# Kernel tuning notes

Hardware: AMD Instinct MI355X
Metric: run time of the kernel (lower is better)

## Reference

```python
import jax, jax.numpy as jnp
import numpy as np

N, E = 100000, 1600000
IN, HID, NCLS = 128, 128, 64


def setup_inputs() -> dict:
    key = jax.random.key(0)
    ks = jax.random.split(key, 8)
    x = jax.random.normal(ks[0], (N, IN), jnp.float32)
    edge_index = jax.random.randint(ks[1], (2, E), 0, N, dtype=jnp.int32)
    s1 = 1.0 / np.sqrt(IN)
    s2 = 1.0 / np.sqrt(HID)
    return {
        "x": x,
        "edge_index": edge_index,
        "Wl1": jax.random.uniform(ks[2], (IN, HID), jnp.float32, -s1, s1),
        "Wr1": jax.random.uniform(ks[3], (IN, HID), jnp.float32, -s1, s1),
        "b1": jnp.zeros((HID,), jnp.float32),
        "Wl2": jax.random.uniform(ks[4], (HID, NCLS), jnp.float32, -s2, s2),
        "Wr2": jax.random.uniform(ks[5], (HID, NCLS), jnp.float32, -s2, s2),
        "b2": jnp.zeros((NCLS,), jnp.float32),
    }


def _sage_conv(x, src, dst, inv_deg, Wl, Wr, b):
    # mean-aggregate neighbor features at each destination node (PyG SAGEConv)
    agg = jax.ops.segment_sum(x[src], dst, num_segments=N)  # [N, d]
    agg = agg * inv_deg[:, None]
    # out = lin_l(mean_j x_j) + lin_r(x_i); bias lives in lin_l
    return agg @ Wl + x @ Wr + b


def reference(x, edge_index, Wl1, Wr1, b1, Wl2, Wr2, b2):
    src, dst = edge_index[0], edge_index[1]
    deg = jax.ops.segment_sum(jnp.ones((E,), jnp.float32), dst, num_segments=N)
    inv_deg = 1.0 / jnp.maximum(deg, 1.0)
    h = _sage_conv(x, src, dst, inv_deg, Wl1, Wr1, b1)
    h = jax.nn.relu(h)
    # dropout is identity at inference (training=False)
    h = _sage_conv(h, src, dst, inv_deg, Wl2, Wr2, b2)
    return jax.nn.log_softmax(h, axis=1)
```

## Files before the change

### kernel.cpp

```cpp
#include <hip/hip_runtime.h>
#include <hip/hip_bf16.h>


typedef __attribute__((ext_vector_type(8))) short short8;
typedef __attribute__((ext_vector_type(4))) float f32x4;
typedef __attribute__((ext_vector_type(2))) float f32x2;

#define NPB 512
#define BCAP 16384
#define CHUNK 8192

__device__ __forceinline__ ushort f2bf(float f) {
    unsigned u = __float_as_uint(f);
    return (ushort)((u + 0x7fff + ((u >> 16) & 1)) >> 16);
}
__device__ __forceinline__ float bflo(unsigned v) { return __uint_as_float(v << 16); }
__device__ __forceinline__ float bfhi(unsigned v) { return __uint_as_float(v & 0xffff0000u); }
__device__ __forceinline__ unsigned pk4bf(float a, float b) {
    unsigned r;
    asm("v_cvt_pk_bf16_f32 %0, %1, %2" : "=v"(r) : "v"(a), "v"(b));
    return r;
}
__device__ __forceinline__ f32x2 shflx2(f32x2 v, int m) {
    f32x2 r; r[0] = __shfl_xor(v[0], m); r[1] = __shfl_xor(v[1], m); return r;
}

__device__ __forceinline__ void wfrag_one(const float* W, ushort* Wf, int i, int COLS) {
    int j = i & 7, m = (i >> 3) & 15, kc = (i >> 7) & 15, ct = i >> 11;
    Wf[i] = f2bf(W[(kc * 8 + j) * COLS + ct * 16 + m]);
}

__global__ void __launch_bounds__(256)
k1_scatter_cvtw(const int* __restrict__ src, const int* __restrict__ dst,
                int* __restrict__ bcount, unsigned* __restrict__ bbuf, int E, int NSC,
                const float* __restrict__ Wl1, const float* __restrict__ Wr1,
                const float* __restrict__ Wl2, const float* __restrict__ Wr2,
                ushort* __restrict__ Wf_l1, ushort* __restrict__ Wf_r1,
                ushort* __restrict__ Wf_l2, ushort* __restrict__ Wf_r2) {
    int tid = threadIdx.x;
    if ((int)blockIdx.x >= NSC) {
        int i = ((int)blockIdx.x - NSC) * 256 + tid;
        if (i < 16384)       wfrag_one(Wl1, Wf_l1, i, 128);
        else if (i < 32768)  wfrag_one(Wr1, Wf_r1, i - 16384, 128);
        else if (i < 40960)  wfrag_one(Wl2, Wf_l2, i - 32768, 64);
        else if (i < 49152)  wfrag_one(Wr2, Wf_r2, i - 40960, 64);
        return;
    }
    __shared__ unsigned entry[CHUNK];
    __shared__ unsigned char ebkt[CHUNK];
    __shared__ int lhist[256], lbase[256], lcur[256];
    lhist[tid] = 0;
    __syncthreads();
    int e0 = blockIdx.x * CHUNK;
    int cnt = min(CHUNK, E - e0);
    int nv = cnt >> 2;
    for (int t = tid; t < nv; t += 256) {
        int4 d4 = ((const int4*)(dst + e0))[t];
        int4 s4 = ((const int4*)(src + e0))[t];
        int i = t * 4;
        int b0 = d4.x >> 9, b1 = d4.y >> 9, b2 = d4.z >> 9, b3 = d4.w >> 9;
        entry[i + 0] = ((unsigned)s4.x << 9) | (unsigned)(d4.x & 511);
        entry[i + 1] = ((unsigned)s4.y << 9) | (unsigned)(d4.y & 511);
        entry[i + 2] = ((unsigned)s4.z << 9) | (unsigned)(d4.z & 511);
        entry[i + 3] = ((unsigned)s4.w << 9) | (unsigned)(d4.w & 511);
        ebkt[i + 0] = (unsigned char)b0; ebkt[i + 1] = (unsigned char)b1;
        ebkt[i + 2] = (unsigned char)b2; ebkt[i + 3] = (unsigned char)b3;
        atomicAdd(&lhist[b0], 1); atomicAdd(&lhist[b1], 1);
        atomicAdd(&lhist[b2], 1); atomicAdd(&lhist[b3], 1);
    }
    for (int i = (nv << 2) + tid; i < cnt; i += 256) {
        int d = dst[e0 + i], s = src[e0 + i];
        int b = d >> 9;
        entry[i] = ((unsigned)s << 9) | (unsigned)(d & 511);
        ebkt[i] = (unsigned char)b;
        atomicAdd(&lhist[b], 1);
    }
    __syncthreads();
    int h = lhist[tid];
    lbase[tid] = (h > 0) ? atomicAdd(&bcount[tid], h) : 0;
    lcur[tid] = 0;
    __syncthreads();
    for (int i = tid; i < cnt; i += 256) {
        int b = ebkt[i];
        int o = atomicAdd(&lcur[b], 1);
        bbuf[(long)b * BCAP + lbase[b] + o] = entry[i];
    }
}

template <int CTOT>
__device__ __forceinline__ void stage_weights(const ushort* __restrict__ Wfl,
                                              const ushort* __restrict__ Wfr,
                                              ushort* dst, int tid) {
    constexpr int HALF = CTOT / 2;
    constexpr int ITERS = (CTOT * 2) / 8192;
#pragma unroll
    for (int r = 0; r < ITERS; ++r) {
        int u = r * 4096 + tid * 8;
        const ushort* s = (u < HALF) ? (Wfl + u) : (Wfr + (u - HALF));
        *(short8*)(dst + u) = *(const short8*)s;
    }
}

template <int COLS, bool F32IN>
__device__ __forceinline__ void proj_body(int bid, int tid,
                            const void* __restrict__ xin,
                            const ushort* __restrict__ Wfl, const ushort* __restrict__ Wfr,
                            const float* __restrict__ bias,
                            unsigned char* __restrict__ p8, ushort* __restrict__ q, int N,
                            ushort* wsm) {
    constexpr int CT = COLS / 16;
    stage_weights<2 * COLS * 128>(Wfl, Wfr, wsm, tid);
    __syncthreads();
    const ushort* Wl = wsm;
    const ushort* Wr = wsm + COLS * 128;

    int wave = tid >> 6, lane = tid & 63;
    int quad = lane >> 4, m = lane & 15;
    long row0 = (long)bid * 128 + wave * 16;
    long node = row0 + m;
    long arow = (node < N) ? node : (N - 1);

    f32x4 accp[CT], accq[CT];
#pragma unroll
    for (int ct = 0; ct < CT; ++ct) { accp[ct] = (f32x4)0.0f; accq[ct] = (f32x4)0.0f; }

#pragma unroll
    for (int kk = 0; kk < 128; kk += 32) {
        short8 b;
        if (F32IN) {
            const float* xf = (const float*)xin + arow * 128 + kk + quad * 8;
            float4 f0 = *(const float4*)xf;
            float4 f1 = *(const float4*)(xf + 4);
            union { short8 s; unsigned u[4]; } bu;
            bu.u[0] = pk4bf(f0.x, f0.y);
            bu.u[1] = pk4bf(f0.z, f0.w);
            bu.u[2] = pk4bf(f1.x, f1.y);
            bu.u[3] = pk4bf(f1.z, f1.w);
            b = bu.s;
        } else {
            b = *(const short8*)((const ushort*)xin + arow * 128 + kk + quad * 8);
        }
        int kc = (kk >> 3) + quad;
#pragma unroll
        for (int ct = 0; ct < CT; ++ct) {
            int boff = ((ct * 16 + kc) * 16 + m) * 8;
            short8 al = *(const short8*)(Wl + boff);
            short8 ar = *(const short8*)(Wr + boff);
            accp[ct] = __builtin_amdgcn_mfma_f32_16x16x32_bf16(al, b, accp[ct], 0, 0, 0);
            accq[ct] = __builtin_amdgcn_mfma_f32_16x16x32_bf16(ar, b, accq[ct], 0, 0, 0);
        }
    }

    if (node <= N) {
        unsigned msk = (node == N) ? 0u : ~0u;
#pragma unroll
        for (int ct = 0; ct < CT; ++ct) {
            int c0 = ct * 16 + quad * 4;
            float4 bv = *(const float4*)(bias + c0);
            float q0 = accq[ct][0] + bv.x, q1 = accq[ct][1] + bv.y;
            float q2 = accq[ct][2] + bv.z, q3 = accq[ct][3] + bv.w;
            unsigned w = (unsigned)__builtin_amdgcn_cvt_pk_fp8_f32(accp[ct][0], accp[ct][1], 0, false);
            w = (unsigned)__builtin_amdgcn_cvt_pk_fp8_f32(accp[ct][2], accp[ct][3], (int)w, true);
            *(unsigned*)(p8 + node * COLS + c0) = w & msk;
            uint2 qw; qw.x = pk4bf(q0, q1) & msk; qw.y = pk4bf(q2, q3) & msk;
            *(uint2*)(q + node * COLS + c0) = qw;
        }
    }
}

__global__ void __launch_bounds__(512, 4)
k2_csr_proj1(const unsigned* __restrict__ bbuf, const int* __restrict__ bcount,
             int* __restrict__ rsd,
             float* __restrict__ inv_deg, int* __restrict__ ssrc, int NBcsr, int N,
             const float* __restrict__ x,
             const ushort* __restrict__ Wfl, const ushort* __restrict__ Wfr,
             const float* __restrict__ bias,
             unsigned char* __restrict__ p8, ushort* __restrict__ q) {
    extern __shared__ char smem[];
    int tid = threadIdx.x;
    if ((int)blockIdx.x >= NBcsr) {
        proj_body<128, true>((int)blockIdx.x - NBcsr, tid, x, Wfl, Wfr, bias, p8, q, N,
                             (ushort*)smem);
        return;
    }
    int* sdeg = (int*)smem;
    int* lcur = sdeg + NPB;
    int* wsum = lcur + NPB;
    int b = blockIdx.x;
    int node0 = b * NPB;
    sdeg[tid] = 0;
    __syncthreads();
    int cnt = bcount[b];
    long base = (long)b * BCAP;
    const unsigned* bb = bbuf + base;
    int nv = cnt >> 2;
    for (int t = tid; t < nv; t += 512) {
        uint4 e = ((const uint4*)bb)[t];
        atomicAdd(&sdeg[e.x & 511], 1);
        atomicAdd(&sdeg[e.y & 511], 1);
        atomicAdd(&sdeg[e.z & 511], 1);
        atomicAdd(&sdeg[e.w & 511], 1);
    }
    for (int i = (nv << 2) + tid; i < cnt; i += 512)
        atomicAdd(&sdeg[bb[i] & 511], 1);
    __syncthreads();
    int lane = tid & 63, wv = tid >> 6;
    int c0 = sdeg[tid];
    int dp = (c0 + 15) & ~15;
    int v = dp;
#pragma unroll
    for (int o = 1; o < 64; o <<= 1) {
        int t = __shfl_up(v, o);
        if (lane >= o) v += t;
    }
    if (lane == 63) wsum[wv] = v;
    __syncthreads();
    int add = 0;
    for (int w = 0; w < wv; ++w) add += wsum[w];
    int rs0 = v + add - dp;
    lcur[tid] = rs0;
    if (node0 + tid < N) {
        int2 rv; rv.x = (int)(base + rs0); rv.y = dp;
        *(int2*)(rsd + 2 * (node0 + tid)) = rv;
        inv_deg[node0 + tid] = 1.0f / (float)(c0 > 1 ? c0 : 1);
    }
    __syncthreads();
    for (int t = tid; t < nv; t += 512) {
        uint4 e = ((const uint4*)bb)[t];
        int p0 = atomicAdd(&lcur[e.x & 511], 1);
        int p1 = atomicAdd(&lcur[e.y & 511], 1);
        int p2 = atomicAdd(&lcur[e.z & 511], 1);
        int p3 = atomicAdd(&lcur[e.w & 511], 1);
        ssrc[base + p0] = (int)(e.x >> 9);
        ssrc[base + p1] = (int)(e.y >> 9);
        ssrc[base + p2] = (int)(e.z >> 9);
        ssrc[base + p3] = (int)(e.w >> 9);
    }
    for (int i = (nv << 2) + tid; i < cnt; i += 512) {
        unsigned w = bb[i];
        int pos = atomicAdd(&lcur[w & 511], 1);
        ssrc[base + pos] = (int)(w >> 9);
    }
    for (int i = c0; i < dp; ++i) ssrc[base + rs0 + i] = N;
    if (tid == 511) {
        int tot = v + add;
        for (int k = 0; k < 16; ++k) ssrc[base + tot + k] = N;
    }
}

__global__ void __launch_bounds__(256)
agg_relu_kernel(const unsigned char* __restrict__ p8,
                const ushort* __restrict__ q,
                const int* __restrict__ ssrc,
                const int* __restrict__ rsd,
                const float* __restrict__ inv_deg,
                ushort* __restrict__ hb, int N) {
    int wave = threadIdx.x >> 6, lane = threadIdx.x & 63;
    int n = blockIdx.x * 4 + wave;
    if (n >= N) return;
    int g = lane >> 4, lm = lane & 15;
    int2 rv = *(const int2*)(rsd + 2 * n);
    int start = rv.x, dp = rv.y;
    float iv = inv_deg[n];
    uint4 qv = make_uint4(0u, 0u, 0u, 0u);
    if (g == 0) qv = *(const uint4*)(q + (long)n * 128 + lm * 8);
    const int* sp = ssrc + start;
    const unsigned char* pb = p8 + lm * 8;
    f32x2 a0 = (f32x2)0.f, a1 = (f32x2)0.f, a2 = (f32x2)0.f, a3 = (f32x2)0.f;
    int4 s = *(const int4*)(sp + 4 * g);
    for (int j = 0; j < dp; j += 16) {
        uint2 v0 = *(const uint2*)(pb + (unsigned)s.x * 128u);
        uint2 v1 = *(const uint2*)(pb + (unsigned)s.y * 128u);
        uint2 v2 = *(const uint2*)(pb + (unsigned)s.z * 128u);
        uint2 v3 = *(const uint2*)(pb + (unsigned)s.w * 128u);
        s = *(const int4*)(sp + j + 16 + 4 * g);
        a0 += __builtin_amdgcn_cvt_pk_f32_fp8((int)v0.x, false);
        a1 += __builtin_amdgcn_cvt_pk_f32_fp8((int)v0.x, true);
        a2 += __builtin_amdgcn_cvt_pk_f32_fp8((int)v0.y, false);
        a3 += __builtin_amdgcn_cvt_pk_f32_fp8((int)v0.y, true);
        a0 += __builtin_amdgcn_cvt_pk_f32_fp8((int)v1.x, false);
        a1 += __builtin_amdgcn_cvt_pk_f32_fp8((int)v1.x, true);
        a2 += __builtin_amdgcn_cvt_pk_f32_fp8((int)v1.y, false);
        a3 += __builtin_amdgcn_cvt_pk_f32_fp8((int)v1.y, true);
        a0 += __builtin_amdgcn_cvt_pk_f32_fp8((int)v2.x, false);
        a1 += __builtin_amdgcn_cvt_pk_f32_fp8((int)v2.x, true);
        a2 += __builtin_amdgcn_cvt_pk_f32_fp8((int)v2.y, false);
        a3 += __builtin_amdgcn_cvt_pk_f32_fp8((int)v2.y, true);
        a0 += __builtin_amdgcn_cvt_pk_f32_fp8((int)v3.x, false);
        a1 += __builtin_amdgcn_cvt_pk_f32_fp8((int)v3.x, true);
        a2 += __builtin_amdgcn_cvt_pk_f32_fp8((int)v3.y, false);
        a3 += __builtin_amdgcn_cvt_pk_f32_fp8((int)v3.y, true);
    }
    a0 += shflx2(a0, 16); a1 += shflx2(a1, 16);
    a2 += shflx2(a2, 16); a3 += shflx2(a3, 16);
    a0 += shflx2(a0, 32); a1 += shflx2(a1, 32);
    a2 += shflx2(a2, 32); a3 += shflx2(a3, 32);
    if (g == 0) {
        float h0 = fmaxf(a0[0] * iv + bflo(qv.x), 0.f);
        float h1 = fmaxf(a0[1] * iv + bfhi(qv.x), 0.f);
        float h2 = fmaxf(a1[0] * iv + bflo(qv.y), 0.f);
        float h3 = fmaxf(a1[1] * iv + bfhi(qv.y), 0.f);
        float h4 = fmaxf(a2[0] * iv + bflo(qv.z), 0.f);
        float h5 = fmaxf(a2[1] * iv + bfhi(qv.z), 0.f);
        float h6 = fmaxf(a3[0] * iv + bflo(qv.w), 0.f);
        float h7 = fmaxf(a3[1] * iv + bfhi(qv.w), 0.f);
        uint4 hw;
        hw.x = pk4bf(h0, h1); hw.y = pk4bf(h2, h3);
        hw.z = pk4bf(h4, h5); hw.w = pk4bf(h6, h7);
        *(uint4*)(hb + (long)n * 128 + lm * 8) = hw;
    }
}

__global__ void __launch_bounds__(512, 4)
proj2_kernel(const ushort* __restrict__ hb,
             const ushort* __restrict__ Wfl, const ushort* __restrict__ Wfr,
             const float* __restrict__ bias,
             unsigned char* __restrict__ u8, ushort* __restrict__ v, int N) {
    __shared__ ushort wsm[2 * 64 * 128];
    proj_body<64, false>((int)blockIdx.x, (int)threadIdx.x, hb, Wfl, Wfr, bias, u8, v, N,
                         wsm);
}

__global__ void __launch_bounds__(256)
agg_lsm_kernel(const unsigned char* __restrict__ u8,
               const ushort* __restrict__ v,
               const int* __restrict__ ssrc,
               const int* __restrict__ rsd,
               const float* __restrict__ inv_deg,
               float* __restrict__ out, int N) {
    int wave = threadIdx.x >> 6, lane = threadIdx.x & 63;
    int n = blockIdx.x * 4 + wave;
    if (n >= N) return;
    int g = lane >> 4, lm = lane & 15;
    int2 rv = *(const int2*)(rsd + 2 * n);
    int start = rv.x, dp = rv.y;
    float iv = inv_deg[n];
    uint2 vv2 = *(const uint2*)(v + (long)n * 64 + lm * 4);
    const int* sp = ssrc + start;
    const unsigned char* ub = u8 + lm * 4;
    f32x2 a0 = (f32x2)0.f, a1 = (f32x2)0.f;
    int4 s = *(const int4*)(sp + 4 * g);
    for (int j = 0; j < dp; j += 16) {
        unsigned v0 = *(const unsigned*)(ub + (unsigned)s.x * 64u);
        unsigned v1 = *(const unsigned*)(ub + (unsigned)s.y * 64u);
        unsigned v2 = *(const unsigned*)(ub + (unsigned)s.z * 64u);
        unsigned v3 = *(const unsigned*)(ub + (unsigned)s.w * 64u);
        s = *(const int4*)(sp + j + 16 + 4 * g);
        a0 += __builtin_amdgcn_cvt_pk_f32_fp8((int)v0, false);
        a1 += __builtin_amdgcn_cvt_pk_f32_fp8((int)v0, true);
        a0 += __builtin_amdgcn_cvt_pk_f32_fp8((int)v1, false);
        a1 += __builtin_amdgcn_cvt_pk_f32_fp8((int)v1, true);
        a0 += __builtin_amdgcn_cvt_pk_f32_fp8((int)v2, false);
        a1 += __builtin_amdgcn_cvt_pk_f32_fp8((int)v2, true);
        a0 += __builtin_amdgcn_cvt_pk_f32_fp8((int)v3, false);
        a1 += __builtin_amdgcn_cvt_pk_f32_fp8((int)v3, true);
    }
    a0 += shflx2(a0, 16); a1 += shflx2(a1, 16);
    a0 += shflx2(a0, 32); a1 += shflx2(a1, 32);

    float z0 = a0[0] * iv + bflo(vv2.x), z1 = a0[1] * iv + bfhi(vv2.x);
    float z2 = a1[0] * iv + bflo(vv2.y), z3 = a1[1] * iv + bfhi(vv2.y);
    float mx = fmaxf(fmaxf(z0, z1), fmaxf(z2, z3));
#pragma unroll
    for (int o = 8; o > 0; o >>= 1) mx = fmaxf(mx, __shfl_xor(mx, o));
    float e = (__expf(z0 - mx) + __expf(z1 - mx)) + (__expf(z2 - mx) + __expf(z3 - mx));
#pragma unroll
    for (int o = 8; o > 0; o >>= 1) e += __shfl_xor(e, o);
    float ls = mx + __logf(e);
    if (g == 0) {
        float4 o0;
        o0.x = z0 - ls; o0.y = z1 - ls; o0.z = z2 - ls; o0.w = z3 - ls;
        *(float4*)(out + (long)n * 64 + lm * 4) = o0;
    }
}

extern "C" void kernel_launch(void* const* d_in, const int* in_sizes, int n_in,
                              void* d_out, int out_size, void* d_ws, size_t ws_size,
                              hipStream_t stream) {
    const float* x   = (const float*)d_in[0];
    const int*   ei  = (const int*)d_in[1];
    const float* Wl1 = (const float*)d_in[2];
    const float* Wr1 = (const float*)d_in[3];
    const float* b1  = (const float*)d_in[4];
    const float* Wl2 = (const float*)d_in[5];
    const float* Wr2 = (const float*)d_in[6];
    const float* b2  = (const float*)d_in[7];

    const int N = in_sizes[0] / 128;
    const int E = in_sizes[1] / 2;
    const int* src = ei;
    const int* dst = ei + E;
    const int NB = (N + NPB - 1) / NPB;
    const int NSC = (E + CHUNK - 1) / CHUNK;

    size_t off = 0;
    auto take = [&](size_t nbytes) -> void* {
        void* ptr = (void*)((char*)d_ws + off);
        off += (nbytes + 255) & ~(size_t)255;
        return ptr;
    };
    int*      bcount    = (int*)take((size_t)NB * 4);
    unsigned* bbuf      = (unsigned*)take((size_t)NB * BCAP * 4);
    int*      rsd       = (int*)take((size_t)N * 8);
    float*    inv_deg   = (float*)take((size_t)N * 4);
    int*      ssrc      = (int*)take((size_t)NB * BCAP * 4);
    unsigned char* p8   = (unsigned char*)take((size_t)(N + 1) * 128);
    ushort*   q         = (ushort*)take((size_t)(N + 1) * 128 * 2);
    ushort*   hb        = (ushort*)take((size_t)N * 128 * 2);
    ushort*   Wf_l1     = (ushort*)take(128 * 128 * 2);
    ushort*   Wf_r1     = (ushort*)take(128 * 128 * 2);
    ushort*   Wf_l2     = (ushort*)take(64 * 128 * 2);
    ushort*   Wf_r2     = (ushort*)take(64 * 128 * 2);
    unsigned char* u8 = p8;
    ushort*        v  = q;
    (void)ws_size; (void)n_in; (void)out_size;

    static bool attr_set = false;
    if (!attr_set) {
        hipFuncSetAttribute((const void*)k2_csr_proj1,
                            hipFuncAttributeMaxDynamicSharedMemorySize, 65536);
        attr_set = true;
    }

    hipMemsetAsync(bcount, 0, (size_t)NB * 4, stream);

    k1_scatter_cvtw<<<NSC + 192, 256, 0, stream>>>(src, dst, bcount, bbuf, E, NSC,
                                                   Wl1, Wr1, Wl2, Wr2,
                                                   Wf_l1, Wf_r1, Wf_l2, Wf_r2);

    int P1 = (N + 127) / 128;
    k2_csr_proj1<<<NB + P1, 512, 65536, stream>>>(bbuf, bcount, rsd, inv_deg,
                                                  ssrc, NB, N, x, Wf_l1, Wf_r1, b1, p8, q);

    agg_relu_kernel<<<(N + 3) / 4, 256, 0, stream>>>(p8, q, ssrc, rsd, inv_deg, hb, N);

    proj2_kernel<<<(N + 127) / 128, 512, 0, stream>>>(hb, Wf_l2, Wf_r2, b2, u8, v, N);
    agg_lsm_kernel<<<(N + 3) / 4, 256, 0, stream>>>(u8, v, ssrc, rsd, inv_deg,
                                                    (float*)d_out, N);
}
```

Baseline: 242.9 us.

## Process two nodes per wave in aggregation kernels and cache bucket edges in LDS

Both aggregation kernels now give each wave two destination nodes and interleave their gathers, so twice as many independent memory requests are in flight per wave, and launch half as many blocks. The CSR build kernel keeps the bucket's edges in shared memory during the degree-count pass, so the scatter pass reads them from LDS instead of global memory again. The cost is more registers per wave, an imbalance tail when the two nodes have different degrees, and LDS space near the 64 KB dynamic limit.

```diff
diff --git a/kernel.cpp b/kernel.cpp
--- a/kernel.cpp
+++ b/kernel.cpp
@@ -186,6 +186,8 @@
     int* sdeg = (int*)smem;
     int* lcur = sdeg + NPB;
     int* wsum = lcur + NPB;
+    unsigned* ecache = (unsigned*)(wsum + 16);
+    const int ECAPV = 3836;
     int b = blockIdx.x;
     int node0 = b * NPB;
     sdeg[tid] = 0;
@@ -194,8 +196,10 @@
     long base = (long)b * BCAP;
     const unsigned* bb = bbuf + base;
     int nv = cnt >> 2;
+    int cnv = min(nv, ECAPV);
     for (int t = tid; t < nv; t += 512) {
         uint4 e = ((const uint4*)bb)[t];
+        if (t < cnv) ((uint4*)ecache)[t] = e;
         atomicAdd(&sdeg[e.x & 511], 1);
         atomicAdd(&sdeg[e.y & 511], 1);
         atomicAdd(&sdeg[e.z & 511], 1);
@@ -225,7 +229,18 @@
         inv_deg[node0 + tid] = 1.0f / (float)(c0 > 1 ? c0 : 1);
     }
     __syncthreads();
-    for (int t = tid; t < nv; t += 512) {
+    for (int t = tid; t < cnv; t += 512) {
+        uint4 e = ((const uint4*)ecache)[t];
+        int p0 = atomicAdd(&lcur[e.x & 511], 1);
+        int p1 = atomicAdd(&lcur[e.y & 511], 1);
+        int p2 = atomicAdd(&lcur[e.z & 511], 1);
+        int p3 = atomicAdd(&lcur[e.w & 511], 1);
+        ssrc[base + p0] = (int)(e.x >> 9);
+        ssrc[base + p1] = (int)(e.y >> 9);
+        ssrc[base + p2] = (int)(e.z >> 9);
+        ssrc[base + p3] = (int)(e.w >> 9);
+    }
+    for (int t = cnv + tid; t < nv; t += 512) {
         uint4 e = ((const uint4*)bb)[t];
         int p0 = atomicAdd(&lcur[e.x & 511], 1);
         int p1 = atomicAdd(&lcur[e.y & 511], 1);
@@ -256,58 +271,155 @@
                 const float* __restrict__ inv_deg,
                 ushort* __restrict__ hb, int N) {
     int wave = threadIdx.x >> 6, lane = threadIdx.x & 63;
-    int n = blockIdx.x * 4 + wave;
-    if (n >= N) return;
+    int nA = blockIdx.x * 8 + wave * 2;
+    if (nA >= N) return;
+    int nB = nA + 1;
+    bool hasB = (nB < N);
     int g = lane >> 4, lm = lane & 15;
-    int2 rv = *(const int2*)(rsd + 2 * n);
-    int start = rv.x, dp = rv.y;
-    float iv = inv_deg[n];
-    uint4 qv = make_uint4(0u, 0u, 0u, 0u);
-    if (g == 0) qv = *(const uint4*)(q + (long)n * 128 + lm * 8);
-    const int* sp = ssrc + start;
+    int2 rvA = *(const int2*)(rsd + 2 * nA);
+    int2 rvB = hasB ? *(const int2*)(rsd + 2 * nB) : make_int2(rvA.x, 0);
+    int dpA = rvA.y, dpB = rvB.y;
+    float ivA = inv_deg[nA];
+    float ivB = hasB ? inv_deg[nB] : 0.f;
+    uint4 qvA = make_uint4(0u,0u,0u,0u), qvB = make_uint4(0u,0u,0u,0u);
+    if (g == 0) {
+        qvA = *(const uint4*)(q + (long)nA * 128 + lm * 8);
+        if (hasB) qvB = *(const uint4*)(q + (long)nB * 128 + lm * 8);
+    }
+    const int* spA = ssrc + rvA.x;
+    const int* spB = ssrc + rvB.x;
     const unsigned char* pb = p8 + lm * 8;
-    f32x2 a0 = (f32x2)0.f, a1 = (f32x2)0.f, a2 = (f32x2)0.f, a3 = (f32x2)0.f;
-    int4 s = *(const int4*)(sp + 4 * g);
-    for (int j = 0; j < dp; j += 16) {
-        uint2 v0 = *(const uint2*)(pb + (unsigned)s.x * 128u);
-        uint2 v1 = *(const uint2*)(pb + (unsigned)s.y * 128u);
-        uint2 v2 = *(const uint2*)(pb + (unsigned)s.z * 128u);
-        uint2 v3 = *(const uint2*)(pb + (unsigned)s.w * 128u);
-        s = *(const int4*)(sp + j + 16 + 4 * g);
-        a0 += __builtin_amdgcn_cvt_pk_f32_fp8((int)v0.x, false);
-        a1 += __builtin_amdgcn_cvt_pk_f32_fp8((int)v0.x, true);
-        a2 += __builtin_amdgcn_cvt_pk_f32_fp8((int)v0.y, false);
-        a3 += __builtin_amdgcn_cvt_pk_f32_fp8((int)v0.y, true);
-        a0 += __builtin_amdgcn_cvt_pk_f32_fp8((int)v1.x, false);
-        a1 += __builtin_amdgcn_cvt_pk_f32_fp8((int)v1.x, true);
-        a2 += __builtin_amdgcn_cvt_pk_f32_fp8((int)v1.y, false);
-        a3 += __builtin_amdgcn_cvt_pk_f32_fp8((int)v1.y, true);
-        a0 += __builtin_amdgcn_cvt_pk_f32_fp8((int)v2.x, false);
-        a1 += __builtin_amdgcn_cvt_pk_f32_fp8((int)v2.x, true);
-        a2 += __builtin_amdgcn_cvt_pk_f32_fp8((int)v2.y, false);
-        a3 += __builtin_amdgcn_cvt_pk_f32_fp8((int)v2.y, true);
-        a0 += __builtin_amdgcn_cvt_pk_f32_fp8((int)v3.x, false);
-        a1 += __builtin_amdgcn_cvt_pk_f32_fp8((int)v3.x, true);
-        a2 += __builtin_amdgcn_cvt_pk_f32_fp8((int)v3.y, false);
-        a3 += __builtin_amdgcn_cvt_pk_f32_fp8((int)v3.y, true);
-    }
-    a0 += shflx2(a0, 16); a1 += shflx2(a1, 16);
-    a2 += shflx2(a2, 16); a3 += shflx2(a3, 16);
-    a0 += shflx2(a0, 32); a1 += shflx2(a1, 32);
-    a2 += shflx2(a2, 32); a3 += shflx2(a3, 32);
+    f32x2 aA0=(f32x2)0.f, aA1=(f32x2)0.f, aA2=(f32x2)0.f, aA3=(f32x2)0.f;
+    f32x2 aB0=(f32x2)0.f, aB1=(f32x2)0.f, aB2=(f32x2)0.f, aB3=(f32x2)0.f;
+    int4 sA = *(const int4*)(spA + 4 * g);
+    int4 sB = *(const int4*)(spB + 4 * g);
+    int dmin = min(dpA, dpB);
+    int j = 0;
+    for (; j < dmin; j += 16) {
+        uint2 a0 = *(const uint2*)(pb + (unsigned)sA.x * 128u);
+        uint2 a1 = *(const uint2*)(pb + (unsigned)sA.y * 128u);
+        uint2 a2 = *(const uint2*)(pb + (unsigned)sA.z * 128u);
+        uint2 a3 = *(const uint2*)(pb + (unsigned)sA.w * 128u);
+        uint2 b0 = *(const uint2*)(pb + (unsigned)sB.x * 128u);
+        uint2 b1 = *(const uint2*)(pb + (unsigned)sB.y * 128u);
+        uint2 b2 = *(const uint2*)(pb + (unsigned)sB.z * 128u);
+        uint2 b3 = *(const uint2*)(pb + (unsigned)sB.w * 128u);
+        sA = *(const int4*)(spA + j + 16 + 4 * g);
+        sB = *(const int4*)(spB + j + 16 + 4 * g);
+        aA0 += __builtin_amdgcn_cvt_pk_f32_fp8((int)a0.x, false);
+        aA1 += __builtin_amdgcn_cvt_pk_f32_fp8((int)a0.x, true);
+        aA2 += __builtin_amdgcn_cvt_pk_f32_fp8((int)a0.y, false);
+        aA3 += __builtin_amdgcn_cvt_pk_f32_fp8((int)a0.y, true);
+        aA0 += __builtin_amdgcn_cvt_pk_f32_fp8((int)a1.x, false);
+        aA1 += __builtin_amdgcn_cvt_pk_f32_fp8((int)a1.x, true);
+        aA2 += __builtin_amdgcn_cvt_pk_f32_fp8((int)a1.y, false);
+        aA3 += __builtin_amdgcn_cvt_pk_f32_fp8((int)a1.y, true);
+        aA0 += __builtin_amdgcn_cvt_pk_f32_fp8((int)a2.x, false);
+        aA1 += __builtin_amdgcn_cvt_pk_f32_fp8((int)a2.x, true);
+        aA2 += __builtin_amdgcn_cvt_pk_f32_fp8((int)a2.y, false);
+        aA3 += __builtin_amdgcn_cvt_pk_f32_fp8((int)a2.y, true);
+        aA0 += __builtin_amdgcn_cvt_pk_f32_fp8((int)a3.x, false);
+        aA1 += __builtin_amdgcn_cvt_pk_f32_fp8((int)a3.x, true);
+        aA2 += __builtin_amdgcn_cvt_pk_f32_fp8((int)a3.y, false);
+        aA3 += __builtin_amdgcn_cvt_pk_f32_fp8((int)a3.y, true);
+        aB0 += __builtin_amdgcn_cvt_pk_f32_fp8((int)b0.x, false);
+        aB1 += __builtin_amdgcn_cvt_pk_f32_fp8((int)b0.x, true);
+        aB2 += __builtin_amdgcn_cvt_pk_f32_fp8((int)b0.y, false);
+        aB3 += __builtin_amdgcn_cvt_pk_f32_fp8((int)b0.y, true);
+        aB0 += __builtin_amdgcn_cvt_pk_f32_fp8((int)b1.x, false);
+        aB1 += __builtin_amdgcn_cvt_pk_f32_fp8((int)b1.x, true);
+        aB2 += __builtin_amdgcn_cvt_pk_f32_fp8((int)b1.y, false);
+        aB3 += __builtin_amdgcn_cvt_pk_f32_fp8((int)b1.y, true);
+        aB0 += __builtin_amdgcn_cvt_pk_f32_fp8((int)b2.x, false);
+        aB1 += __builtin_amdgcn_cvt_pk_f32_fp8((int)b2.x, true);
+        aB2 += __builtin_amdgcn_cvt_pk_f32_fp8((int)b2.y, false);
+        aB3 += __builtin_amdgcn_cvt_pk_f32_fp8((int)b2.y, true);
+        aB0 += __builtin_amdgcn_cvt_pk_f32_fp8((int)b3.x, false);
+        aB1 += __builtin_amdgcn_cvt_pk_f32_fp8((int)b3.x, true);
+        aB2 += __builtin_amdgcn_cvt_pk_f32_fp8((int)b3.y, false);
+        aB3 += __builtin_amdgcn_cvt_pk_f32_fp8((int)b3.y, true);
+    }
+    for (; j < dpA; j += 16) {
+        uint2 a0 = *(const uint2*)(pb + (unsigned)sA.x * 128u);
+        uint2 a1 = *(const uint2*)(pb + (unsigned)sA.y * 128u);
+        uint2 a2 = *(const uint2*)(pb + (unsigned)sA.z * 128u);
+        uint2 a3 = *(const uint2*)(pb + (unsigned)sA.w * 128u);
+        sA = *(const int4*)(spA + j + 16 + 4 * g);
+        aA0 += __builtin_amdgcn_cvt_pk_f32_fp8((int)a0.x, false);
+        aA1 += __builtin_amdgcn_cvt_pk_f32_fp8((int)a0.x, true);
+        aA2 += __builtin_amdgcn_cvt_pk_f32_fp8((int)a0.y, false);
+        aA3 += __builtin_amdgcn_cvt_pk_f32_fp8((int)a0.y, true);
+        aA0 += __builtin_amdgcn_cvt_pk_f32_fp8((int)a1.x, false);
+        aA1 += __builtin_amdgcn_cvt_pk_f32_fp8((int)a1.x, true);
+        aA2 += __builtin_amdgcn_cvt_pk_f32_fp8((int)a1.y, false);
+        aA3 += __builtin_amdgcn_cvt_pk_f32_fp8((int)a1.y, true);
+        aA0 += __builtin_amdgcn_cvt_pk_f32_fp8((int)a2.x, false);
+        aA1 += __builtin_amdgcn_cvt_pk_f32_fp8((int)a2.x, true);
+        aA2 += __builtin_amdgcn_cvt_pk_f32_fp8((int)a2.y, false);
+        aA3 += __builtin_amdgcn_cvt_pk_f32_fp8((int)a2.y, true);
+        aA0 += __builtin_amdgcn_cvt_pk_f32_fp8((int)a3.x, false);
+        aA1 += __builtin_amdgcn_cvt_pk_f32_fp8((int)a3.x, true);
+        aA2 += __builtin_amdgcn_cvt_pk_f32_fp8((int)a3.y, false);
+        aA3 += __builtin_amdgcn_cvt_pk_f32_fp8((int)a3.y, true);
+    }
+    for (; j < dpB; j += 16) {
+        uint2 b0 = *(const uint2*)(pb + (unsigned)sB.x * 128u);
+        uint2 b1 = *(const uint2*)(pb + (unsigned)sB.y * 128u);
+        uint2 b2 = *(const uint2*)(pb + (unsigned)sB.z * 128u);
+        uint2 b3 = *(const uint2*)(pb + (unsigned)sB.w * 128u);
+        sB = *(const int4*)(spB + j + 16 + 4 * g);
+        aB0 += __builtin_amdgcn_cvt_pk_f32_fp8((int)b0.x, false);
+        aB1 += __builtin_amdgcn_cvt_pk_f32_fp8((int)b0.x, true);
+        aB2 += __builtin_amdgcn_cvt_pk_f32_fp8((int)b0.y, false);
+        aB3 += __builtin_amdgcn_cvt_pk_f32_fp8((int)b0.y, true);
+        aB0 += __builtin_amdgcn_cvt_pk_f32_fp8((int)b1.x, false);
+        aB1 += __builtin_amdgcn_cvt_pk_f32_fp8((int)b1.x, true);
+        aB2 += __builtin_amdgcn_cvt_pk_f32_fp8((int)b1.y, false);
+        aB3 += __builtin_amdgcn_cvt_pk_f32_fp8((int)b1.y, true);
+        aB0 += __builtin_amdgcn_cvt_pk_f32_fp8((int)b2.x, false);
+        aB1 += __builtin_amdgcn_cvt_pk_f32_fp8((int)b2.x, true);
+        aB2 += __builtin_amdgcn_cvt_pk_f32_fp8((int)b2.y, false);
+        aB3 += __builtin_amdgcn_cvt_pk_f32_fp8((int)b2.y, true);
+        aB0 += __builtin_amdgcn_cvt_pk_f32_fp8((int)b3.x, false);
+        aB1 += __builtin_amdgcn_cvt_pk_f32_fp8((int)b3.x, true);
+        aB2 += __builtin_amdgcn_cvt_pk_f32_fp8((int)b3.y, false);
+        aB3 += __builtin_amdgcn_cvt_pk_f32_fp8((int)b3.y, true);
+    }
+    aA0 += shflx2(aA0, 16); aA1 += shflx2(aA1, 16);
+    aA2 += shflx2(aA2, 16); aA3 += shflx2(aA3, 16);
+    aB0 += shflx2(aB0, 16); aB1 += shflx2(aB1, 16);
+    aB2 += shflx2(aB2, 16); aB3 += shflx2(aB3, 16);
+    aA0 += shflx2(aA0, 32); aA1 += shflx2(aA1, 32);
+    aA2 += shflx2(aA2, 32); aA3 += shflx2(aA3, 32);
+    aB0 += shflx2(aB0, 32); aB1 += shflx2(aB1, 32);
+    aB2 += shflx2(aB2, 32); aB3 += shflx2(aB3, 32);
     if (g == 0) {
-        float h0 = fmaxf(a0[0] * iv + bflo(qv.x), 0.f);
-        float h1 = fmaxf(a0[1] * iv + bfhi(qv.x), 0.f);
-        float h2 = fmaxf(a1[0] * iv + bflo(qv.y), 0.f);
-        float h3 = fmaxf(a1[1] * iv + bfhi(qv.y), 0.f);
-        float h4 = fmaxf(a2[0] * iv + bflo(qv.z), 0.f);
-        float h5 = fmaxf(a2[1] * iv + bfhi(qv.z), 0.f);
-        float h6 = fmaxf(a3[0] * iv + bflo(qv.w), 0.f);
-        float h7 = fmaxf(a3[1] * iv + bfhi(qv.w), 0.f);
+        float h0 = fmaxf(aA0[0] * ivA + bflo(qvA.x), 0.f);
+        float h1 = fmaxf(aA0[1] * ivA + bfhi(qvA.x), 0.f);
+        float h2 = fmaxf(aA1[0] * ivA + bflo(qvA.y), 0.f);
+        float h3 = fmaxf(aA1[1] * ivA + bfhi(qvA.y), 0.f);
+        float h4 = fmaxf(aA2[0] * ivA + bflo(qvA.z), 0.f);
+        float h5 = fmaxf(aA2[1] * ivA + bfhi(qvA.z), 0.f);
+        float h6 = fmaxf(aA3[0] * ivA + bflo(qvA.w), 0.f);
+        float h7 = fmaxf(aA3[1] * ivA + bfhi(qvA.w), 0.f);
         uint4 hw;
         hw.x = pk4bf(h0, h1); hw.y = pk4bf(h2, h3);
         hw.z = pk4bf(h4, h5); hw.w = pk4bf(h6, h7);
-        *(uint4*)(hb + (long)n * 128 + lm * 8) = hw;
+        *(uint4*)(hb + (long)nA * 128 + lm * 8) = hw;
+        if (hasB) {
+            float g0 = fmaxf(aB0[0] * ivB + bflo(qvB.x), 0.f);
+            float g1 = fmaxf(aB0[1] * ivB + bfhi(qvB.x), 0.f);
+            float g2 = fmaxf(aB1[0] * ivB + bflo(qvB.y), 0.f);
+            float g3 = fmaxf(aB1[1] * ivB + bfhi(qvB.y), 0.f);
+            float g4 = fmaxf(aB2[0] * ivB + bflo(qvB.z), 0.f);
+            float g5 = fmaxf(aB2[1] * ivB + bfhi(qvB.z), 0.f);
+            float g6 = fmaxf(aB3[0] * ivB + bflo(qvB.w), 0.f);
+            float g7 = fmaxf(aB3[1] * ivB + bfhi(qvB.w), 0.f);
+            uint4 gw;
+            gw.x = pk4bf(g0, g1); gw.y = pk4bf(g2, g3);
+            gw.z = pk4bf(g4, g5); gw.w = pk4bf(g6, g7);
+            *(uint4*)(hb + (long)nB * 128 + lm * 8) = gw;
+        }
     }
 }
 
@@ -329,48 +441,118 @@
                const float* __restrict__ inv_deg,
                float* __restrict__ out, int N) {
     int wave = threadIdx.x >> 6, lane = threadIdx.x & 63;
-    int n = blockIdx.x * 4 + wave;
-    if (n >= N) return;
+    int nA = blockIdx.x * 8 + wave * 2;
+    if (nA >= N) return;
+    int nB = nA + 1;
+    bool hasB = (nB < N);
     int g = lane >> 4, lm = lane & 15;
-    int2 rv = *(const int2*)(rsd + 2 * n);
-    int start = rv.x, dp = rv.y;
-    float iv = inv_deg[n];
-    uint2 vv2 = *(const uint2*)(v + (long)n * 64 + lm * 4);
-    const int* sp = ssrc + start;
+    int2 rvA = *(const int2*)(rsd + 2 * nA);
+    int2 rvB = hasB ? *(const int2*)(rsd + 2 * nB) : make_int2(rvA.x, 0);
+    int dpA = rvA.y, dpB = rvB.y;
+    float ivA = inv_deg[nA];
+    float ivB = hasB ? inv_deg[nB] : 0.f;
+    uint2 vvA = *(const uint2*)(v + (long)nA * 64 + lm * 4);
+    uint2 vvB = hasB ? *(const uint2*)(v + (long)nB * 64 + lm * 4) : make_uint2(0u,0u);
+    const int* spA = ssrc + rvA.x;
+    const int* spB = ssrc + rvB.x;
     const unsigned char* ub = u8 + lm * 4;
-    f32x2 a0 = (f32x2)0.f, a1 = (f32x2)0.f;
-    int4 s = *(const int4*)(sp + 4 * g);
-    for (int j = 0; j < dp; j += 16) {
-        unsigned v0 = *(const unsigned*)(ub + (unsigned)s.x * 64u);
-        unsigned v1 = *(const unsigned*)(ub + (unsigned)s.y * 64u);
-        unsigned v2 = *(const unsigned*)(ub + (unsigned)s.z * 64u);
-        unsigned v3 = *(const unsigned*)(ub + (unsigned)s.w * 64u);
-        s = *(const int4*)(sp + j + 16 + 4 * g);
-        a0 += __builtin_amdgcn_cvt_pk_f32_fp8((int)v0, false);
-        a1 += __builtin_amdgcn_cvt_pk_f32_fp8((int)v0, true);
-        a0 += __builtin_amdgcn_cvt_pk_f32_fp8((int)v1, false);
-        a1 += __builtin_amdgcn_cvt_pk_f32_fp8((int)v1, true);
-        a0 += __builtin_amdgcn_cvt_pk_f32_fp8((int)v2, false);
-        a1 += __builtin_amdgcn_cvt_pk_f32_fp8((int)v2, true);
-        a0 += __builtin_amdgcn_cvt_pk_f32_fp8((int)v3, false);
-        a1 += __builtin_amdgcn_cvt_pk_f32_fp8((int)v3, true);
-    }
-    a0 += shflx2(a0, 16); a1 += shflx2(a1, 16);
-    a0 += shflx2(a0, 32); a1 += shflx2(a1, 32);
-
-    float z0 = a0[0] * iv + bflo(vv2.x), z1 = a0[1] * iv + bfhi(vv2.x);
-    float z2 = a1[0] * iv + bflo(vv2.y), z3 = a1[1] * iv + bfhi(vv2.y);
-    float mx = fmaxf(fmaxf(z0, z1), fmaxf(z2, z3));
-#pragma unroll
-    for (int o = 8; o > 0; o >>= 1) mx = fmaxf(mx, __shfl_xor(mx, o));
-    float e = (__expf(z0 - mx) + __expf(z1 - mx)) + (__expf(z2 - mx) + __expf(z3 - mx));
-#pragma unroll
-    for (int o = 8; o > 0; o >>= 1) e += __shfl_xor(e, o);
-    float ls = mx + __logf(e);
+    f32x2 aA0=(f32x2)0.f, aA1=(f32x2)0.f, aB0=(f32x2)0.f, aB1=(f32x2)0.f;
+    int4 sA = *(const int4*)(spA + 4 * g);
+    int4 sB = *(const int4*)(spB + 4 * g);
+    int dmin = min(dpA, dpB);
+    int j = 0;
+    for (; j < dmin; j += 16) {
+        unsigned a0 = *(const unsigned*)(ub + (unsigned)sA.x * 64u);
+        unsigned a1 = *(const unsigned*)(ub + (unsigned)sA.y * 64u);
+        unsigned a2 = *(const unsigned*)(ub + (unsigned)sA.z * 64u);
+        unsigned a3 = *(const unsigned*)(ub + (unsigned)sA.w * 64u);
+        unsigned b0 = *(const unsigned*)(ub + (unsigned)sB.x * 64u);
+        unsigned b1 = *(const unsigned*)(ub + (unsigned)sB.y * 64u);
+        unsigned b2 = *(const unsigned*)(ub + (unsigned)sB.z * 64u);
+        unsigned b3 = *(const unsigned*)(ub + (unsigned)sB.w * 64u);
+        sA = *(const int4*)(spA + j + 16 + 4 * g);
+        sB = *(const int4*)(spB + j + 16 + 4 * g);
+        aA0 += __builtin_amdgcn_cvt_pk_f32_fp8((int)a0, false);
+        aA1 += __builtin_amdgcn_cvt_pk_f32_fp8((int)a0, true);
+        aA0 += __builtin_amdgcn_cvt_pk_f32_fp8((int)a1, false);
+        aA1 += __builtin_amdgcn_cvt_pk_f32_fp8((int)a1, true);
+        aA0 += __builtin_amdgcn_cvt_pk_f32_fp8((int)a2, false);
+        aA1 += __builtin_amdgcn_cvt_pk_f32_fp8((int)a2, true);
+        aA0 += __builtin_amdgcn_cvt_pk_f32_fp8((int)a3, false);
+        aA1 += __builtin_amdgcn_cvt_pk_f32_fp8((int)a3, true);
+        aB0 += __builtin_amdgcn_cvt_pk_f32_fp8((int)b0, false);
+        aB1 += __builtin_amdgcn_cvt_pk_f32_fp8((int)b0, true);
+        aB0 += __builtin_amdgcn_cvt_pk_f32_fp8((int)b1, false);
+        aB1 += __builtin_amdgcn_cvt_pk_f32_fp8((int)b1, true);
+        aB0 += __builtin_amdgcn_cvt_pk_f32_fp8((int)b2, false);
+        aB1 += __builtin_amdgcn_cvt_pk_f32_fp8((int)b2, true);
+        aB0 += __builtin_amdgcn_cvt_pk_f32_fp8((int)b3, false);
+        aB1 += __builtin_amdgcn_cvt_pk_f32_fp8((int)b3, true);
+    }
+    for (; j < dpA; j += 16) {
+        unsigned a0 = *(const unsigned*)(ub + (unsigned)sA.x * 64u);
+        unsigned a1 = *(const unsigned*)(ub + (unsigned)sA.y * 64u);
+        unsigned a2 = *(const unsigned*)(ub + (unsigned)sA.z * 64u);
+        unsigned a3 = *(const unsigned*)(ub + (unsigned)sA.w * 64u);
+        sA = *(const int4*)(spA + j + 16 + 4 * g);
+        aA0 += __builtin_amdgcn_cvt_pk_f32_fp8((int)a0, false);
+        aA1 += __builtin_amdgcn_cvt_pk_f32_fp8((int)a0, true);
+        aA0 += __builtin_amdgcn_cvt_pk_f32_fp8((int)a1, false);
+        aA1 += __builtin_amdgcn_cvt_pk_f32_fp8((int)a1, true);
+        aA0 += __builtin_amdgcn_cvt_pk_f32_fp8((int)a2, false);
+        aA1 += __builtin_amdgcn_cvt_pk_f32_fp8((int)a2, true);
+        aA0 += __builtin_amdgcn_cvt_pk_f32_fp8((int)a3, false);
+        aA1 += __builtin_amdgcn_cvt_pk_f32_fp8((int)a3, true);
+    }
+    for (; j < dpB; j += 16) {
+        unsigned b0 = *(const unsigned*)(ub + (unsigned)sB.x * 64u);
+        unsigned b1 = *(const unsigned*)(ub + (unsigned)sB.y * 64u);
+        unsigned b2 = *(const unsigned*)(ub + (unsigned)sB.z * 64u);
+        unsigned b3 = *(const unsigned*)(ub + (unsigned)sB.w * 64u);
+        sB = *(const int4*)(spB + j + 16 + 4 * g);
+        aB0 += __builtin_amdgcn_cvt_pk_f32_fp8((int)b0, false);
+        aB1 += __builtin_amdgcn_cvt_pk_f32_fp8((int)b0, true);
+        aB0 += __builtin_amdgcn_cvt_pk_f32_fp8((int)b1, false);
+        aB1 += __builtin_amdgcn_cvt_pk_f32_fp8((int)b1, true);
+        aB0 += __builtin_amdgcn_cvt_pk_f32_fp8((int)b2, false);
+        aB1 += __builtin_amdgcn_cvt_pk_f32_fp8((int)b2, true);
+        aB0 += __builtin_amdgcn_cvt_pk_f32_fp8((int)b3, false);
+        aB1 += __builtin_amdgcn_cvt_pk_f32_fp8((int)b3, true);
+    }
+    aA0 += shflx2(aA0, 16); aA1 += shflx2(aA1, 16);
+    aB0 += shflx2(aB0, 16); aB1 += shflx2(aB1, 16);
+    aA0 += shflx2(aA0, 32); aA1 += shflx2(aA1, 32);
+    aB0 += shflx2(aB0, 32); aB1 += shflx2(aB1, 32);
+
+    float zA0 = aA0[0] * ivA + bflo(vvA.x), zA1 = aA0[1] * ivA + bfhi(vvA.x);
+    float zA2 = aA1[0] * ivA + bflo(vvA.y), zA3 = aA1[1] * ivA + bfhi(vvA.y);
+    float zB0 = aB0[0] * ivB + bflo(vvB.x), zB1 = aB0[1] * ivB + bfhi(vvB.x);
+    float zB2 = aB1[0] * ivB + bflo(vvB.y), zB3 = aB1[1] * ivB + bfhi(vvB.y);
+    float mA = fmaxf(fmaxf(zA0, zA1), fmaxf(zA2, zA3));
+    float mB = fmaxf(fmaxf(zB0, zB1), fmaxf(zB2, zB3));
+#pragma unroll
+    for (int o = 8; o > 0; o >>= 1) {
+        mA = fmaxf(mA, __shfl_xor(mA, o));
+        mB = fmaxf(mB, __shfl_xor(mB, o));
+    }
+    float eA = (__expf(zA0 - mA) + __expf(zA1 - mA)) + (__expf(zA2 - mA) + __expf(zA3 - mA));
+    float eB = (__expf(zB0 - mB) + __expf(zB1 - mB)) + (__expf(zB2 - mB) + __expf(zB3 - mB));
+#pragma unroll
+    for (int o = 8; o > 0; o >>= 1) {
+        eA += __shfl_xor(eA, o);
+        eB += __shfl_xor(eB, o);
+    }
+    float lsA = mA + __logf(eA);
+    float lsB = mB + __logf(eB);
     if (g == 0) {
-        float4 o0;
-        o0.x = z0 - ls; o0.y = z1 - ls; o0.z = z2 - ls; o0.w = z3 - ls;
-        *(float4*)(out + (long)n * 64 + lm * 4) = o0;
+        float4 oA;
+        oA.x = zA0 - lsA; oA.y = zA1 - lsA; oA.z = zA2 - lsA; oA.w = zA3 - lsA;
+        *(float4*)(out + (long)nA * 64 + lm * 4) = oA;
+        if (hasB) {
+            float4 oB;
+            oB.x = zB0 - lsB; oB.y = zB1 - lsB; oB.z = zB2 - lsB; oB.w = zB3 - lsB;
+            *(float4*)(out + (long)nB * 64 + lm * 4) = oB;
+        }
     }
 }
 
@@ -432,9 +614,9 @@
     k2_csr_proj1<<<NB + P1, 512, 65536, stream>>>(bbuf, bcount, rsd, inv_deg,
                                                   ssrc, NB, N, x, Wf_l1, Wf_r1, b1, p8, q);
 
-    agg_relu_kernel<<<(N + 3) / 4, 256, 0, stream>>>(p8, q, ssrc, rsd, inv_deg, hb, N);
+    agg_relu_kernel<<<(N + 7) / 8, 256, 0, stream>>>(p8, q, ssrc, rsd, inv_deg, hb, N);
 
     proj2_kernel<<<(N + 127) / 128, 512, 0, stream>>>(hb, Wf_l2, Wf_r2, b2, u8, v, N);
-    agg_lsm_kernel<<<(N + 3) / 4, 256, 0, stream>>>(u8, v, ssrc, rsd, inv_deg,
+    agg_lsm_kernel<<<(N + 7) / 8, 256, 0, stream>>>(u8, v, ssrc, rsd, inv_deg,
                                                     (float*)d_out, N);
 }
```

New measurement: 242.4 us. No clear change (-0.2%).

## Persist proj1 blocks, cache CSR edges in LDS, use packed f32 adds

Applied to the files above, without the earlier changes.

The projection part of k2 becomes a persistent grid of 316 blocks. Each block stages the bf16 weights into shared memory once and then loops over row tiles, instead of restaging per 128-row tile. The CSR build blocks keep up to about 15K edges in the unused LDS during the degree pass, so the scatter pass reads them from LDS instead of re-reading global memory. Both aggregation kernels now accumulate with an explicit v_pk_add_f32 in inline asm. The risks are less scheduling freedom for the compiler around the asm and load imbalance across the persistent blocks.

```diff
diff --git a/kernel.cpp b/kernel.cpp
--- a/kernel.cpp
+++ b/kernel.cpp
@@ -19,6 +19,11 @@
 __device__ __forceinline__ unsigned pk4bf(float a, float b) {
     unsigned r;
     asm("v_cvt_pk_bf16_f32 %0, %1, %2" : "=v"(r) : "v"(a), "v"(b));
+    return r;
+}
+__device__ __forceinline__ f32x2 pkadd(f32x2 a, f32x2 b) {
+    f32x2 r;
+    asm("v_pk_add_f32 %0, %1, %2" : "=v"(r) : "v"(a), "v"(b));
     return r;
 }
 __device__ __forceinline__ f32x2 shflx2(f32x2 v, int m) {
@@ -102,18 +107,12 @@
 }
 
 template <int COLS, bool F32IN>
-__device__ __forceinline__ void proj_body(int bid, int tid,
+__device__ __forceinline__ void proj_tile(int bid, int tid,
                             const void* __restrict__ xin,
-                            const ushort* __restrict__ Wfl, const ushort* __restrict__ Wfr,
+                            const ushort* Wl, const ushort* Wr,
                             const float* __restrict__ bias,
-                            unsigned char* __restrict__ p8, ushort* __restrict__ q, int N,
-                            ushort* wsm) {
+                            unsigned char* __restrict__ p8, ushort* __restrict__ q, int N) {
     constexpr int CT = COLS / 16;
-    stage_weights<2 * COLS * 128>(Wfl, Wfr, wsm, tid);
-    __syncthreads();
-    const ushort* Wl = wsm;
-    const ushort* Wr = wsm + COLS * 128;
-
     int wave = tid >> 6, lane = tid & 63;
     int quad = lane >> 4, m = lane & 15;
     long row0 = (long)bid * 128 + wave * 16;
@@ -171,7 +170,8 @@
 __global__ void __launch_bounds__(512, 4)
 k2_csr_proj1(const unsigned* __restrict__ bbuf, const int* __restrict__ bcount,
              int* __restrict__ rsd,
-             float* __restrict__ inv_deg, int* __restrict__ ssrc, int NBcsr, int N,
+             float* __restrict__ inv_deg, int* __restrict__ ssrc,
+             int NBcsr, int PGRID, int NT, int N,
              const float* __restrict__ x,
              const ushort* __restrict__ Wfl, const ushort* __restrict__ Wfr,
              const float* __restrict__ bias,
@@ -179,13 +179,18 @@
     extern __shared__ char smem[];
     int tid = threadIdx.x;
     if ((int)blockIdx.x >= NBcsr) {
-        proj_body<128, true>((int)blockIdx.x - NBcsr, tid, x, Wfl, Wfr, bias, p8, q, N,
-                             (ushort*)smem);
+        ushort* wsm = (ushort*)smem;
+        stage_weights<2 * 128 * 128>(Wfl, Wfr, wsm, tid);
+        __syncthreads();
+        for (int t = (int)blockIdx.x - NBcsr; t < NT; t += PGRID)
+            proj_tile<128, true>(t, tid, x, wsm, wsm + 128 * 128, bias, p8, q, N);
         return;
     }
     int* sdeg = (int*)smem;
     int* lcur = sdeg + NPB;
     int* wsum = lcur + NPB;
+    unsigned* ecache = (unsigned*)(wsum + 16);
+    const int ECAPV = 3836;
     int b = blockIdx.x;
     int node0 = b * NPB;
     sdeg[tid] = 0;
@@ -194,8 +199,10 @@
     long base = (long)b * BCAP;
     const unsigned* bb = bbuf + base;
     int nv = cnt >> 2;
+    int cnv = min(nv, ECAPV);
     for (int t = tid; t < nv; t += 512) {
         uint4 e = ((const uint4*)bb)[t];
+        if (t < cnv) ((uint4*)ecache)[t] = e;
         atomicAdd(&sdeg[e.x & 511], 1);
         atomicAdd(&sdeg[e.y & 511], 1);
         atomicAdd(&sdeg[e.z & 511], 1);
@@ -225,7 +232,18 @@
         inv_deg[node0 + tid] = 1.0f / (float)(c0 > 1 ? c0 : 1);
     }
     __syncthreads();
-    for (int t = tid; t < nv; t += 512) {
+    for (int t = tid; t < cnv; t += 512) {
+        uint4 e = ((const uint4*)ecache)[t];
+        int p0 = atomicAdd(&lcur[e.x & 511], 1);
+        int p1 = atomicAdd(&lcur[e.y & 511], 1);
+        int p2 = atomicAdd(&lcur[e.z & 511], 1);
+        int p3 = atomicAdd(&lcur[e.w & 511], 1);
+        ssrc[base + p0] = (int)(e.x >> 9);
+        ssrc[base + p1] = (int)(e.y >> 9);
+        ssrc[base + p2] = (int)(e.z >> 9);
+        ssrc[base + p3] = (int)(e.w >> 9);
+    }
+    for (int t = cnv + tid; t < nv; t += 512) {
         uint4 e = ((const uint4*)bb)[t];
         int p0 = atomicAdd(&lcur[e.x & 511], 1);
         int p1 = atomicAdd(&lcur[e.y & 511], 1);
@@ -274,27 +292,27 @@
         uint2 v2 = *(const uint2*)(pb + (unsigned)s.z * 128u);
         uint2 v3 = *(const uint2*)(pb + (unsigned)s.w * 128u);
         s = *(const int4*)(sp + j + 16 + 4 * g);
-        a0 += __builtin_amdgcn_cvt_pk_f32_fp8((int)v0.x, false);
-        a1 += __builtin_amdgcn_cvt_pk_f32_fp8((int)v0.x, true);
-        a2 += __builtin_amdgcn_cvt_pk_f32_fp8((int)v0.y, false);
-        a3 += __builtin_amdgcn_cvt_pk_f32_fp8((int)v0.y, true);
-        a0 += __builtin_amdgcn_cvt_pk_f32_fp8((int)v1.x, false);
-        a1 += __builtin_amdgcn_cvt_pk_f32_fp8((int)v1.x, true);
-        a2 += __builtin_amdgcn_cvt_pk_f32_fp8((int)v1.y, false);
-        a3 += __builtin_amdgcn_cvt_pk_f32_fp8((int)v1.y, true);
-        a0 += __builtin_amdgcn_cvt_pk_f32_fp8((int)v2.x, false);
-        a1 += __builtin_amdgcn_cvt_pk_f32_fp8((int)v2.x, true);
-        a2 += __builtin_amdgcn_cvt_pk_f32_fp8((int)v2.y, false);
-        a3 += __builtin_amdgcn_cvt_pk_f32_fp8((int)v2.y, true);
-        a0 += __builtin_amdgcn_cvt_pk_f32_fp8((int)v3.x, false);
-        a1 += __builtin_amdgcn_cvt_pk_f32_fp8((int)v3.x, true);
-        a2 += __builtin_amdgcn_cvt_pk_f32_fp8((int)v3.y, false);
-        a3 += __builtin_amdgcn_cvt_pk_f32_fp8((int)v3.y, true);
-    }
-    a0 += shflx2(a0, 16); a1 += shflx2(a1, 16);
-    a2 += shflx2(a2, 16); a3 += shflx2(a3, 16);
-    a0 += shflx2(a0, 32); a1 += shflx2(a1, 32);
-    a2 += shflx2(a2, 32); a3 += shflx2(a3, 32);
+        a0 = pkadd(a0, __builtin_amdgcn_cvt_pk_f32_fp8((int)v0.x, false));
+        a1 = pkadd(a1, __builtin_amdgcn_cvt_pk_f32_fp8((int)v0.x, true));
+        a2 = pkadd(a2, __builtin_amdgcn_cvt_pk_f32_fp8((int)v0.y, false));
+        a3 = pkadd(a3, __builtin_amdgcn_cvt_pk_f32_fp8((int)v0.y, true));
+        a0 = pkadd(a0, __builtin_amdgcn_cvt_pk_f32_fp8((int)v1.x, false));
+        a1 = pkadd(a1, __builtin_amdgcn_cvt_pk_f32_fp8((int)v1.x, true));
+        a2 = pkadd(a2, __builtin_amdgcn_cvt_pk_f32_fp8((int)v1.y, false));
+        a3 = pkadd(a3, __builtin_amdgcn_cvt_pk_f32_fp8((int)v1.y, true));
+        a0 = pkadd(a0, __builtin_amdgcn_cvt_pk_f32_fp8((int)v2.x, false));
+        a1 = pkadd(a1, __builtin_amdgcn_cvt_pk_f32_fp8((int)v2.x, true));
+        a2 = pkadd(a2, __builtin_amdgcn_cvt_pk_f32_fp8((int)v2.y, false));
+        a3 = pkadd(a3, __builtin_amdgcn_cvt_pk_f32_fp8((int)v2.y, true));
+        a0 = pkadd(a0, __builtin_amdgcn_cvt_pk_f32_fp8((int)v3.x, false));
+        a1 = pkadd(a1, __builtin_amdgcn_cvt_pk_f32_fp8((int)v3.x, true));
+        a2 = pkadd(a2, __builtin_amdgcn_cvt_pk_f32_fp8((int)v3.y, false));
+        a3 = pkadd(a3, __builtin_amdgcn_cvt_pk_f32_fp8((int)v3.y, true));
+    }
+    a0 = pkadd(a0, shflx2(a0, 16)); a1 = pkadd(a1, shflx2(a1, 16));
+    a2 = pkadd(a2, shflx2(a2, 16)); a3 = pkadd(a3, shflx2(a3, 16));
+    a0 = pkadd(a0, shflx2(a0, 32)); a1 = pkadd(a1, shflx2(a1, 32));
+    a2 = pkadd(a2, shflx2(a2, 32)); a3 = pkadd(a3, shflx2(a3, 32));
     if (g == 0) {
         float h0 = fmaxf(a0[0] * iv + bflo(qv.x), 0.f);
         float h1 = fmaxf(a0[1] * iv + bfhi(qv.x), 0.f);
@@ -317,8 +335,10 @@
              const float* __restrict__ bias,
              unsigned char* __restrict__ u8, ushort* __restrict__ v, int N) {
     __shared__ ushort wsm[2 * 64 * 128];
-    proj_body<64, false>((int)blockIdx.x, (int)threadIdx.x, hb, Wfl, Wfr, bias, u8, v, N,
-                         wsm);
+    stage_weights<2 * 64 * 128>(Wfl, Wfr, wsm, (int)threadIdx.x);
+    __syncthreads();
+    proj_tile<64, false>((int)blockIdx.x, (int)threadIdx.x, hb, wsm, wsm + 64 * 128,
+                         bias, u8, v, N);
 }
 
 __global__ void __launch_bounds__(256)
@@ -346,17 +366,17 @@
         unsigned v2 = *(const unsigned*)(ub + (unsigned)s.z * 64u);
         unsigned v3 = *(const unsigned*)(ub + (unsigned)s.w * 64u);
         s = *(const int4*)(sp + j + 16 + 4 * g);
-        a0 += __builtin_amdgcn_cvt_pk_f32_fp8((int)v0, false);
-        a1 += __builtin_amdgcn_cvt_pk_f32_fp8((int)v0, true);
-        a0 += __builtin_amdgcn_cvt_pk_f32_fp8((int)v1, false);
-        a1 += __builtin_amdgcn_cvt_pk_f32_fp8((int)v1, true);
-        a0 += __builtin_amdgcn_cvt_pk_f32_fp8((int)v2, false);
-        a1 += __builtin_amdgcn_cvt_pk_f32_fp8((int)v2, true);
-        a0 += __builtin_amdgcn_cvt_pk_f32_fp8((int)v3, false);
-        a1 += __builtin_amdgcn_cvt_pk_f32_fp8((int)v3, true);
-    }
-    a0 += shflx2(a0, 16); a1 += shflx2(a1, 16);
-    a0 += shflx2(a0, 32); a1 += shflx2(a1, 32);
+        a0 = pkadd(a0, __builtin_amdgcn_cvt_pk_f32_fp8((int)v0, false));
+        a1 = pkadd(a1, __builtin_amdgcn_cvt_pk_f32_fp8((int)v0, true));
+        a0 = pkadd(a0, __builtin_amdgcn_cvt_pk_f32_fp8((int)v1, false));
+        a1 = pkadd(a1, __builtin_amdgcn_cvt_pk_f32_fp8((int)v1, true));
+        a0 = pkadd(a0, __builtin_amdgcn_cvt_pk_f32_fp8((int)v2, false));
+        a1 = pkadd(a1, __builtin_amdgcn_cvt_pk_f32_fp8((int)v2, true));
+        a0 = pkadd(a0, __builtin_amdgcn_cvt_pk_f32_fp8((int)v3, false));
+        a1 = pkadd(a1, __builtin_amdgcn_cvt_pk_f32_fp8((int)v3, true));
+    }
+    a0 = pkadd(a0, shflx2(a0, 16)); a1 = pkadd(a1, shflx2(a1, 16));
+    a0 = pkadd(a0, shflx2(a0, 32)); a1 = pkadd(a1, shflx2(a1, 32));
 
     float z0 = a0[0] * iv + bflo(vv2.x), z1 = a0[1] * iv + bfhi(vv2.x);
     float z2 = a1[0] * iv + bflo(vv2.y), z3 = a1[1] * iv + bfhi(vv2.y);
@@ -428,9 +448,11 @@
                                                    Wl1, Wr1, Wl2, Wr2,
                                                    Wf_l1, Wf_r1, Wf_l2, Wf_r2);
 
-    int P1 = (N + 127) / 128;
-    k2_csr_proj1<<<NB + P1, 512, 65536, stream>>>(bbuf, bcount, rsd, inv_deg,
-                                                  ssrc, NB, N, x, Wf_l1, Wf_r1, b1, p8, q);
+    const int PGRID = 316;
+    const int NT = (N + 127) / 128;
+    k2_csr_proj1<<<NB + PGRID, 512, 65536, stream>>>(bbuf, bcount, rsd, inv_deg, ssrc,
+                                                     NB, PGRID, NT, N, x,
+                                                     Wf_l1, Wf_r1, b1, p8, q);
 
     agg_relu_kernel<<<(N + 3) / 4, 256, 0, stream>>>(p8, q, ssrc, rsd, inv_deg, hb, N);
 
```

Result: no change. 246.9 us (+1.7%).
